# Kernel tuning notes

Hardware: AMD Instinct MI355X
Metric: run time of the kernel (lower is better)

The kernel has to match this reference:

```python
import jax, jax.numpy as jnp
import numpy as np

B, LEN, D, N = 512, 128, 96, 128   # batch, time steps, obs dim, latent dim
NBLOCKS = 5                        # iResNet blocks in encoder/decoder


def expm_fixed(M, squarings=6, order=12):
    """Differentiable matrix exponential: scaling-and-squaring + Taylor-Horner.
    Equivalent to torch.matrix_exp for the well-conditioned skew-symmetric
    A*dt kernels used here (||A*dt|| << 2^squarings)."""
    M = M / (2.0 ** squarings)
    I = jnp.eye(M.shape[-1], dtype=M.dtype)
    P = I
    for k in range(order, 0, -1):  # Horner: I + M(I + M/2(I + ...))
        P = I + (M @ P) / k
    for _ in range(squarings):
        P = P @ P
    return P


def setup_inputs() -> dict:
    key = jax.random.key(0)
    ks = jax.random.split(key, 16)
    # strictly increasing timestamps shared across the batch
    T = jnp.cumsum(0.01 + 0.15 * jax.random.uniform(ks[0], (LEN,), dtype=jnp.float32))
    X = jax.random.normal(ks[1], (B, LEN, D), dtype=jnp.float32)
    mask = jax.random.bernoulli(ks[2], 0.5, (B, LEN, D))  # True = observed
    # skew-symmetric system kernel (kernel_initialization='skew-symmetric')
    W = jax.random.normal(ks[3], (N, N), dtype=jnp.float32) / np.sqrt(N)
    A = 0.5 * (W - W.T)
    # linear embedding d->n and projection n->d
    W_emb = jax.random.normal(ks[4], (N, D), dtype=jnp.float32) / np.sqrt(D)
    b_emb = jnp.zeros((N,), jnp.float32)
    W_proj = jax.random.normal(ks[5], (D, N), dtype=jnp.float32) / np.sqrt(N)
    b_proj = jnp.zeros((D,), jnp.float32)
    # iResNet encoder/decoder: 5 residual blocks of Linear->ReLU->Linear,
    # weights scaled small to mimic the spectral-norm contraction constraint
    cs = 0.5 / np.sqrt(N)
    enc_W1 = jax.random.normal(ks[6], (NBLOCKS, N, N), dtype=jnp.float32) * cs
    enc_b1 = jnp.zeros((NBLOCKS, N), jnp.float32)
    enc_W2 = jax.random.normal(ks[7], (NBLOCKS, N, N), dtype=jnp.float32) * cs
    enc_b2 = jnp.zeros((NBLOCKS, N), jnp.float32)
    dec_W1 = jax.random.normal(ks[8], (NBLOCKS, N, N), dtype=jnp.float32) * cs
    dec_b1 = jnp.zeros((NBLOCKS, N), jnp.float32)
    dec_W2 = jax.random.normal(ks[9], (NBLOCKS, N, N), dtype=jnp.float32) * cs
    dec_b2 = jnp.zeros((NBLOCKS, N), jnp.float32)
    # GRUCell filter: input = concat([xtilde, mask]) (2D features), hidden = D
    s = 1.0 / np.sqrt(D)
    W_ih = jax.random.uniform(ks[10], (3 * D, 2 * D), jnp.float32, -s, s)
    W_hh = jax.random.uniform(ks[11], (3 * D, D), jnp.float32, -s, s)
    b_ih = jax.random.uniform(ks[12], (3 * D,), jnp.float32, -s, s)
    b_hh = jax.random.uniform(ks[13], (3 * D,), jnp.float32, -s, s)
    return {"T": T, "X": X, "mask": mask, "A": A,
            "W_emb": W_emb, "b_emb": b_emb, "W_proj": W_proj, "b_proj": b_proj,
            "enc_W1": enc_W1, "enc_b1": enc_b1, "enc_W2": enc_W2, "enc_b2": enc_b2,
            "dec_W1": dec_W1, "dec_b1": dec_b1, "dec_W2": dec_W2, "dec_b2": dec_b2,
            "W_ih": W_ih, "W_hh": W_hh, "b_ih": b_ih, "b_hh": b_hh}


def reference(T, X, mask, A, W_emb, b_emb, W_proj, b_proj,
              enc_W1, enc_b1, enc_W2, enc_b2,
              dec_W1, dec_b1, dec_W2, dec_b2,
              W_ih, W_hh, b_ih, b_hh):
    def resnet(z, Ws1, bs1, Ws2, bs2):
        for i in range(NBLOCKS):  # fixed small depth
            z = z + jax.nn.relu(z @ Ws1[i].T + bs1[i]) @ Ws2[i].T + bs2[i]
        return z

    def gru(x, h):  # torch.nn.GRUCell math
        gi = x @ W_ih.T + b_ih
        gh = h @ W_hh.T + b_hh
        ir, iz, inn = jnp.split(gi, 3, axis=-1)
        hr, hz, hn = jnp.split(gh, 3, axis=-1)
        r = jax.nn.sigmoid(ir + hr)
        zg = jax.nn.sigmoid(iz + hz)
        ng = jnp.tanh(inn + r * hn)
        return (1.0 - zg) * ng + zg * h

    embed = lambda x: x @ W_emb.T + b_emb
    project = lambda z: z @ W_proj.T + b_proj

    dt = jnp.concatenate([jnp.zeros((1,), T.dtype), jnp.diff(T)])  # (LEN,)
    Xs = jnp.moveaxis(X, 1, 0)      # (LEN, B, D)
    Ms = jnp.moveaxis(mask, 1, 0)   # (LEN, B, D)

    # initial latent state from zero estimate
    z0 = resnet(embed(jnp.zeros((B, D), X.dtype)), enc_W1, enc_b1, enc_W2, enc_b2)

    def step(z, inp):
        dti, xi, mi = inp
        expAdt = expm_fixed(A * dti)                         # (N, N)
        zhat_pre = z @ expAdt.T                              # ODE propagate
        xhat_pre = project(resnet(zhat_pre, dec_W1, dec_b1, dec_W2, dec_b2))
        xtilde = jnp.where(mi, xi, xhat_pre)                 # impute unobserved
        u = jnp.concatenate([xtilde, mi.astype(xi.dtype)], axis=-1)  # concat_mask
        xhat_post = gru(u, xhat_pre)                         # filter update
        z_next = resnet(embed(xhat_post), enc_W1, enc_b1, enc_W2, enc_b2)
        return z_next, xhat_post

    _, Xhat = jax.lax.scan(step, z0, (dt, Xs, Ms))
    return jnp.moveaxis(Xhat, 0, 1)  # (B, LEN, D)
```

## Files before the change

### kernel.cpp

```cpp
#include <hip/hip_runtime.h>
#include <hip/hip_bf16.h>


#define NBATCH 512
#define TLEN 128
#define DDIM 96
#define NDIM 128
#define NBLK 5
#define TAYLOR 8
#define A_STRIDE_E 136

typedef unsigned short u16;
typedef unsigned int u32;

__device__ __forceinline__ float bf2f(u16 u){ union{u32 i; float f;} v; v.i=((u32)u)<<16; return v.f; }
__device__ __forceinline__ float lo2f(u32 w){ union{u32 i; float f;} v; v.i=w<<16; return v.f; }
__device__ __forceinline__ float hi2f(u32 w){ union{u32 i; float f;} v; v.i=w&0xFFFF0000u; return v.f; }
__device__ __forceinline__ u16 f2bf(float x){ union{float f;u32 i;} v; v.f=x; u32 r=v.i+0x7FFF+((v.i>>16)&1); return (u16)(r>>16); }

template<int FM>
__device__ __forceinline__ float ldf(const void* p, int i){
  if constexpr (FM==1) return ((const float*)p)[i];
  else return bf2f(((const u16*)p)[i]);
}

#define OEB1 0
#define OEB2 640
#define ODB1 1280
#define ODB2 1920
#define OBEMB 2560
#define OBPROJ 2688
#define OBIH 2784
#define OBHH 3072
#define NBIAS 3360

struct __align__(16) SMState {
  float e[NDIM];
  float V0[NDIM];
  float V1[NDIM];
  float zh[NDIM];
  float h[NDIM];
  float xpre[DDIM];
  float u[2*DDIM];
  float gi[3*DDIM];
  float gh[3*DDIM];
  float xpost[DDIM];
};

__global__ __launch_bounds__(256, 1)
void expm_kernel(const void* Tp, const void* Ap, u16* Ews)
{
  __shared__ int sf;
  __shared__ __align__(16) u16 Ash2[NDIM*A_STRIDE_E];
  __shared__ __align__(16) float V[2][64*132];
  const int tid = threadIdx.x;
  if (tid==0){
    int all0=1;
    for (int k=0;k<8;k++) all0 &= (((const u32*)Ap)[129*k]==0u);
    sf = all0;
  }
  __syncthreads();
  if (sf) return;

  const int t = blockIdx.x >> 1, half = blockIdx.x & 1;
  float dtv = 0.f;
  if (t>0) dtv = bf2f(((const u16*)Tp)[t]) - bf2f(((const u16*)Tp)[t-1]);
  {
    const uint4* src = (const uint4*)Ap;
    for (int i=tid;i<2048;i+=256){
      const int row=i>>4, c=i&15;
      *(uint4*)((char*)Ash2 + 2*(size_t)row*A_STRIDE_E + 16*c) = src[i];
    }
  }
  const int c2 = tid & 31, rh = tid >> 5;
  const int j0r = rh*16;
  const int lc0 = 2*c2, lc1 = lc0+1;
  const int gc0 = half*64 + lc0, gc1 = gc0+1;

  float acc0[16], acc1[16];
#pragma unroll
  for (int jj=0;jj<16;jj++){
    const int kk = j0r+jj;
    const float i0 = (kk==gc0)?1.f:0.f, i1 = (kk==gc1)?1.f:0.f;
    acc0[jj]=i0; acc1[jj]=i1;
    V[0][lc0*132+kk]=i0; V[0][lc1*132+kk]=i1;
  }
  __syncthreads();
  int cur=0;
#pragma unroll 1
  for (int k=1;k<=8;k++){
    const float sc = dtv/(float)k;
    float o0[16], o1[16];
#pragma unroll
    for (int jj=0;jj<16;jj++){ o0[jj]=0.f; o1[jj]=0.f; }
#pragma unroll 1
    for (int kb=0;kb<16;kb++){
      const float4 va0 = *(const float4*)&V[cur][lc0*132+kb*8];
      const float4 vb0 = *(const float4*)&V[cur][lc0*132+kb*8+4];
      const float4 va1 = *(const float4*)&V[cur][lc1*132+kb*8];
      const float4 vb1 = *(const float4*)&V[cur][lc1*132+kb*8+4];
      const float v0[8]={va0.x,va0.y,va0.z,va0.w,vb0.x,vb0.y,vb0.z,vb0.w};
      const float v1[8]={va1.x,va1.y,va1.z,va1.w,vb1.x,vb1.y,vb1.z,vb1.w};
#pragma unroll
      for (int jj=0;jj<16;jj++){
        const int j = j0r+jj;
        const uint4 w = *(const uint4*)((const char*)Ash2 + 2*(size_t)j*A_STRIDE_E + 16*kb);
        float f;
        f=lo2f(w.x); o0[jj]=fmaf(f,v0[0],o0[jj]); o1[jj]=fmaf(f,v1[0],o1[jj]);
        f=hi2f(w.x); o0[jj]=fmaf(f,v0[1],o0[jj]); o1[jj]=fmaf(f,v1[1],o1[jj]);
        f=lo2f(w.y); o0[jj]=fmaf(f,v0[2],o0[jj]); o1[jj]=fmaf(f,v1[2],o1[jj]);
        f=hi2f(w.y); o0[jj]=fmaf(f,v0[3],o0[jj]); o1[jj]=fmaf(f,v1[3],o1[jj]);
        f=lo2f(w.z); o0[jj]=fmaf(f,v0[4],o0[jj]); o1[jj]=fmaf(f,v1[4],o1[jj]);
        f=hi2f(w.z); o0[jj]=fmaf(f,v0[5],o0[jj]); o1[jj]=fmaf(f,v1[5],o1[jj]);
        f=lo2f(w.w); o0[jj]=fmaf(f,v0[6],o0[jj]); o1[jj]=fmaf(f,v1[6],o1[jj]);
        f=hi2f(w.w); o0[jj]=fmaf(f,v0[7],o0[jj]); o1[jj]=fmaf(f,v1[7],o1[jj]);
      }
    }
    __syncthreads();
#pragma unroll
    for (int jj=0;jj<16;jj++){
      const int j=j0r+jj;
      const float s0=o0[jj]*sc, s1=o1[jj]*sc;
      acc0[jj]+=s0; acc1[jj]+=s1;
      V[cur^1][lc0*132+j]=s0; V[cur^1][lc1*132+j]=s1;
    }
    __syncthreads();
    cur^=1;
  }
#pragma unroll
  for (int jj=0;jj<16;jj++){
    const int j=j0r+jj;
    const u32 pk = (u32)f2bf(acc0[jj]) | ((u32)f2bf(acc1[jj])<<16);
    *((u32*)(Ews + (size_t)t*NDIM*NDIM + (size_t)j*NDIM + gc0)) = pk;
  }
}

template<int FM, int S, int NO, bool WL, class EPI>
__device__ __forceinline__ void mv(const void* __restrict__ Wg, const u16* __restrict__ Wl,
                                   const int ldw, const float* __restrict__ in,
                                   const int kq, const int j0, EPI epi)
{
  constexpr int NC = S/8;
  constexpr int P = (NO+127)/128;
  constexpr bool full = (NO%128==0);
  float a[S];
  {
    const float* p = in + 8*kq;
#pragma unroll
    for (int ci=0; ci<NC; ci++){
      float4 v0 = *(const float4*)(p + 32*ci);
      float4 v1 = *(const float4*)(p + 32*ci + 4);
      a[8*ci+0]=v0.x; a[8*ci+1]=v0.y; a[8*ci+2]=v0.z; a[8*ci+3]=v0.w;
      a[8*ci+4]=v1.x; a[8*ci+5]=v1.y; a[8*ci+6]=v1.z; a[8*ci+7]=v1.w;
    }
  }
#pragma unroll
  for (int pp=0; pp<P; pp++){
    const int j = pp*128 + j0;
    const bool act = full || (j < NO);
    float ac0=0.f, ac1=0.f, ac2=0.f, ac3=0.f;
    if (act){
      if constexpr (WL){
        const char* wr = (const char*)Wl + 2*(size_t)j*A_STRIDE_E + 16*kq;
#pragma unroll
        for (int ci=0; ci<NC; ci++){
          const uint4 w = *(const uint4*)(wr + 64*ci);
          float f;
          f=lo2f(w.x); ac0=fmaf(f,a[8*ci+0],ac0);
          f=hi2f(w.x); ac1=fmaf(f,a[8*ci+1],ac1);
          f=lo2f(w.y); ac2=fmaf(f,a[8*ci+2],ac2);
          f=hi2f(w.y); ac3=fmaf(f,a[8*ci+3],ac3);
          f=lo2f(w.z); ac0=fmaf(f,a[8*ci+4],ac0);
          f=hi2f(w.z); ac1=fmaf(f,a[8*ci+5],ac1);
          f=lo2f(w.w); ac2=fmaf(f,a[8*ci+6],ac2);
          f=hi2f(w.w); ac3=fmaf(f,a[8*ci+7],ac3);
        }
      } else if constexpr (FM==1){
        const float* wr = (const float*)Wg + (size_t)j*ldw + 8*kq;
#pragma unroll
        for (int ci=0; ci<NC; ci++){
          const float4 w0 = *(const float4*)(wr + 32*ci);
          const float4 w1 = *(const float4*)(wr + 32*ci + 4);
          ac0=fmaf(w0.x,a[8*ci+0],ac0); ac1=fmaf(w0.y,a[8*ci+1],ac1);
          ac2=fmaf(w0.z,a[8*ci+2],ac2); ac3=fmaf(w0.w,a[8*ci+3],ac3);
          ac0=fmaf(w1.x,a[8*ci+4],ac0); ac1=fmaf(w1.y,a[8*ci+5],ac1);
          ac2=fmaf(w1.z,a[8*ci+6],ac2); ac3=fmaf(w1.w,a[8*ci+7],ac3);
        }
      } else {
        const u16* wr = (const u16*)Wg + (size_t)j*ldw + 8*kq;
#pragma unroll
        for (int ci=0; ci<NC; ci++){
          const uint4 w = *(const uint4*)(wr + 32*ci);
          float f;
          f=lo2f(w.x); ac0=fmaf(f,a[8*ci+0],ac0);
          f=hi2f(w.x); ac1=fmaf(f,a[8*ci+1],ac1);
          f=lo2f(w.y); ac2=fmaf(f,a[8*ci+2],ac2);
          f=hi2f(w.y); ac3=fmaf(f,a[8*ci+3],ac3);
          f=lo2f(w.z); ac0=fmaf(f,a[8*ci+4],ac0);
          f=hi2f(w.z); ac1=fmaf(f,a[8*ci+5],ac1);
          f=lo2f(w.w); ac2=fmaf(f,a[8*ci+6],ac2);
          f=hi2f(w.w); ac3=fmaf(f,a[8*ci+7],ac3);
        }
      }
    }
    float acc = (ac0+ac1)+(ac2+ac3);
    acc += __shfl_xor(acc,1,64); acc += __shfl_xor(acc,2,64);
    if (act && kq==0) epi(j, acc);
  }
  __syncthreads();
}

template<int FM>
__device__ __forceinline__ void stage_b(const void* src, float* dst, int n, int tid){
  for (int i=tid;i<n;i+=512) dst[i] = ldf<FM>(src,i);
}

template<int FM>
__device__ __forceinline__ void run_all(
    SMState& sm, float* smb, u16* Ash, const int mode, const int useE,
    const void* Tp, const void* Xp, const void* Mp, const void* Ap,
    const void* Wemb, const void* bemb, const void* Wproj, const void* bproj,
    const void* eW1, const void* eb1, const void* eW2, const void* eb2,
    const void* dW1, const void* db1, const void* dW2, const void* db2,
    const void* Wih, const void* Whh, const void* bih, const void* bhh,
    const u16* Ep, void* Out)
{
  const int tid  = threadIdx.x;
  const int lane = tid & 63;
  const int kq   = lane & 3;
  const int j0   = (tid>>6)*16 + (lane>>2);
  const int r0   = blockIdx.x;
  constexpr int WB = NDIM*NDIM*(FM?4:2);

  stage_b<FM>(eb1, smb+OEB1, NBLK*NDIM, tid);
  stage_b<FM>(eb2, smb+OEB2, NBLK*NDIM, tid);
  stage_b<FM>(db1, smb+ODB1, NBLK*NDIM, tid);
  stage_b<FM>(db2, smb+ODB2, NBLK*NDIM, tid);
  stage_b<FM>(bemb, smb+OBEMB, NDIM, tid);
  stage_b<FM>(bproj, smb+OBPROJ, DDIM, tid);
  stage_b<FM>(bih, smb+OBIH, 3*DDIM, tid);
  stage_b<FM>(bhh, smb+OBHH, 3*DDIM, tid);
  if (FM==0 && !useE){
    const uint4* src = (const uint4*)Ap;
    for (int i=tid;i<2048;i+=512){
      const int row=i>>4, c=i&15;
      *(uint4*)((char*)Ash + 2*(size_t)row*A_STRIDE_E + 16*c) = src[i];
    }
  }
  __syncthreads();

  if (tid < NDIM) sm.e[tid] = smb[OBEMB+tid];
  __syncthreads();
#pragma unroll 1
  for (int ib=0; ib<NBLK; ib++){
    const void* W1 = (const char*)eW1 + (size_t)ib*WB;
    const void* W2 = (const char*)eW2 + (size_t)ib*WB;
    const int bo = ib*NDIM;
    mv<FM,32,128,false>(W1, nullptr, NDIM, sm.e, kq, j0, [&](int j,float s){
      sm.h[j]=fmaxf(s+smb[OEB1+bo+j],0.f); });
    mv<FM,32,128,false>(W2, nullptr, NDIM, sm.h, kq, j0, [&](int j,float s){
      sm.e[j]+=s+smb[OEB2+bo+j]; });
  }

#pragma unroll 1
  for (int t=0; t<TLEN; t++){
    float xv_r = 0.f; int m_r = 0;
    if (tid < DDIM){
      const size_t idx = (size_t)r0*TLEN*DDIM + (size_t)t*DDIM + tid;
      if      (mode==0) m_r = ((const u16*)Mp)[idx] != 0;
      else if (mode==1) m_r = ((const u32*)Mp)[idx] != 0;
      else if (mode==2) m_r = ((const unsigned char*)Mp)[idx] != 0;
      else              m_r = ((const int*)Mp)[idx] != 0;
      xv_r = ldf<FM>(Xp, (int)idx);
    }

    if (FM==0 && useE){
      const u16* Et = Ep + (size_t)t*NDIM*NDIM;
      mv<0,32,128,false>(Et, nullptr, NDIM, sm.e, kq, j0, [&](int j,float s){
        sm.zh[j]=s; });
    } else {
      float dtv = 0.f;
      if (t>0) dtv = ldf<FM>(Tp,t) - ldf<FM>(Tp,t-1);
      if (tid < NDIM){ const float z=sm.e[tid]; sm.V0[tid]=z; sm.zh[tid]=z; }
      __syncthreads();
#pragma unroll 1
      for (int k=1;k<=TAYLOR;k++){
        const float sc = dtv/(float)k;
        const float* Vin = (k&1)?sm.V0:sm.V1;
        float*      Vout = (k&1)?sm.V1:sm.V0;
        if constexpr (FM==0){
          mv<0,32,128,true>(nullptr, Ash, NDIM, Vin, kq, j0, [&](int j,float s){
            const float v=s*sc; Vout[j]=v; sm.zh[j]+=v; });
        } else {
          mv<1,32,128,false>(Ap, nullptr, NDIM, Vin, kq, j0, [&](int j,float s){
            const float v=s*sc; Vout[j]=v; sm.zh[j]+=v; });
        }
      }
    }

#pragma unroll 1
    for (int ib=0; ib<NBLK; ib++){
      const void* W1 = (const char*)dW1 + (size_t)ib*WB;
      const void* W2 = (const char*)dW2 + (size_t)ib*WB;
      const int bo = ib*NDIM;
      mv<FM,32,128,false>(W1, nullptr, NDIM, sm.zh, kq, j0, [&](int j,float s){
        sm.h[j]=fmaxf(s+smb[ODB1+bo+j],0.f); });
      mv<FM,32,128,false>(W2, nullptr, NDIM, sm.h, kq, j0, [&](int j,float s){
        sm.zh[j]+=s+smb[ODB2+bo+j]; });
    }

    mv<FM,32,96,false>(Wproj, nullptr, NDIM, sm.zh, kq, j0, [&](int j,float s){
      sm.xpre[j]=s+smb[OBPROJ+j]; });

    if (tid < DDIM){
      sm.u[tid]      = m_r ? xv_r : sm.xpre[tid];
      sm.u[DDIM+tid] = m_r ? 1.f : 0.f;
    }
    __syncthreads();

    mv<FM,48,288,false>(Wih, nullptr, 2*DDIM, sm.u, kq, j0, [&](int j,float s){
      sm.gi[j]=s+smb[OBIH+j]; });
    mv<FM,24,288,false>(Whh, nullptr, DDIM, sm.xpre, kq, j0, [&](int j,float s){
      sm.gh[j]=s+smb[OBHH+j]; });

    if (tid < DDIM){
      const int d = tid;
      const float ir=sm.gi[d], iz=sm.gi[DDIM+d], in_=sm.gi[2*DDIM+d];
      const float hr=sm.gh[d], hz=sm.gh[DDIM+d], hn=sm.gh[2*DDIM+d];
      const float rg = 1.f/(1.f+__expf(-(ir+hr)));
      const float zg = 1.f/(1.f+__expf(-(iz+hz)));
      const float ag = in_ + rg*hn;
      const float e2 = __expf(2.f*ag);
      const float ng = 1.f - 2.f/(e2+1.f);
      const float xp = sm.xpre[d];
      const float xq = (1.f-zg)*ng + zg*xp;
      sm.xpost[d] = xq;
      const size_t idx = (size_t)r0*TLEN*DDIM + (size_t)t*DDIM + d;
      if constexpr (FM==1) ((float*)Out)[idx] = xq;
      else ((__hip_bfloat16*)Out)[idx] = __float2bfloat16(xq);
    }
    __syncthreads();

    mv<FM,24,128,false>(Wemb, nullptr, DDIM, sm.xpost, kq, j0, [&](int j,float s){
      sm.e[j]=s+smb[OBEMB+j]; });

#pragma unroll 1
    for (int ib=0; ib<NBLK; ib++){
      const void* W1 = (const char*)eW1 + (size_t)ib*WB;
      const void* W2 = (const char*)eW2 + (size_t)ib*WB;
      const int bo = ib*NDIM;
      mv<FM,32,128,false>(W1, nullptr, NDIM, sm.e, kq, j0, [&](int j,float s){
        sm.h[j]=fmaxf(s+smb[OEB1+bo+j],0.f); });
      mv<FM,32,128,false>(W2, nullptr, NDIM, sm.h, kq, j0, [&](int j,float s){
        sm.e[j]+=s+smb[OEB2+bo+j]; });
    }
  }
}

__global__ __launch_bounds__(512, 4)
void linode_kernel(const void* Tp, const void* Xp, const void* Mp, const void* Ap,
                   const void* Wemb, const void* bemb, const void* Wproj, const void* bproj,
                   const void* eW1, const void* eb1, const void* eW2, const void* eb2,
                   const void* dW1, const void* db1, const void* dW2, const void* db2,
                   const void* Wih, const void* Whh, const void* bih, const void* bhh,
                   const u16* Ep, const int useE, void* Out)
{
  __shared__ SMState sm;
  __shared__ float smb[NBIAS];
  __shared__ __align__(16) u16 Ash[NDIM*A_STRIDE_E];
  __shared__ int s_f[4];
  const int tid = threadIdx.x;

  if (tid < 4) s_f[tid] = 0;
  __syncthreads();
  if (tid == 0){
    int all0 = 1;
    for (int k=0;k<8;k++) all0 &= (((const u32*)Ap)[129*k] == 0u);
    s_f[3] = all0;
  }
  {
    const u32* mw = (const u32*)Mp;
    int fb=0, ff=0, fg=0;
    for (int i=tid;i<2048;i+=512){
      const u32 w = mw[i];
      if (w == 0x3F803F80u) fb = 1;
      if ((w&0xFFFFu)==0x3F80u || (w>>16)==0x3F80u) ff = 1;
      if (w > 1u) fg = 1;
    }
    if (fb) atomicOr(&s_f[0],1);
    if (ff) atomicOr(&s_f[1],1);
    if (fg) atomicOr(&s_f[2],1);
  }
  __syncthreads();
  const int mode = s_f[0] ? 0 : (s_f[1] ? 1 : (s_f[2] ? 2 : 3));
  const int f32m = s_f[3];
  __syncthreads();

  if (f32m)
    run_all<1>(sm, smb, Ash, mode, useE, Tp, Xp, Mp, Ap, Wemb, bemb, Wproj, bproj,
               eW1, eb1, eW2, eb2, dW1, db1, dW2, db2, Wih, Whh, bih, bhh, Ep, Out);
  else
    run_all<0>(sm, smb, Ash, mode, useE, Tp, Xp, Mp, Ap, Wemb, bemb, Wproj, bproj,
               eW1, eb1, eW2, eb2, dW1, db1, dW2, db2, Wih, Whh, bih, bhh, Ep, Out);
}

extern "C" void kernel_launch(void* const* d_in, const int* in_sizes, int n_in,
                              void* d_out, int out_size, void* d_ws, size_t ws_size,
                              hipStream_t stream)
{
  (void)in_sizes; (void)n_in; (void)out_size;
  const int useE = (ws_size >= (size_t)TLEN*NDIM*NDIM*2) ? 1 : 0;
  if (useE)
    hipLaunchKernelGGL(expm_kernel, dim3(2*TLEN), dim3(256), 0, stream,
                       d_in[0], d_in[3], (u16*)d_ws);
  hipLaunchKernelGGL(linode_kernel, dim3(NBATCH), dim3(512), 0, stream,
                     d_in[0], d_in[1], d_in[2], d_in[3],
                     d_in[4], d_in[5], d_in[6], d_in[7],
                     d_in[8], d_in[9], d_in[10], d_in[11],
                     d_in[12], d_in[13], d_in[14], d_in[15],
                     d_in[16], d_in[17], d_in[18], d_in[19],
                     (const u16*)d_ws, useE, d_out);
}
```

Before: 5.207 ms.

## Add software-pipelined bf16 path that prefetches next layer weights into registers

Adds a dedicated run_pipe path for bf16 inputs with the precomputed expm workspace. Inside each per-step chain of matvecs it loads the next layer's weight fragment into registers while the current dot product and reduction run, hiding global/L2 load latency behind compute. The GRU gate matvecs are computed directly with several outputs per thread, and the bias staging moves ahead of the path dispatch. This costs extra registers and duplicated code, and it assumes bf16 weights and a workspace large enough for the expm buffer.

```diff
diff --git a/kernel.cpp b/kernel.cpp
--- a/kernel.cpp
+++ b/kernel.cpp
@@ -132,6 +132,216 @@
     const int j=j0r+jj;
     const u32 pk = (u32)f2bf(acc0[jj]) | ((u32)f2bf(acc1[jj])<<16);
     *((u32*)(Ews + (size_t)t*NDIM*NDIM + (size_t)j*NDIM + gc0)) = pk;
+  }
+}
+
+template<int NC>
+__device__ __forceinline__ void wload(uint4* wp, const u16* W, int ldw_e, int j, int kq){
+  const u16* wr = W + (size_t)j*ldw_e + 8*kq;
+#pragma unroll
+  for (int ci=0; ci<NC; ci++) wp[ci] = *(const uint4*)(wr + 32*ci);
+}
+template<int S>
+__device__ __forceinline__ void aload(float* a, const float* in, int kq){
+  const float* p = in + 8*kq;
+#pragma unroll
+  for (int ci=0; ci<S/8; ci++){
+    float4 v0 = *(const float4*)(p + 32*ci);
+    float4 v1 = *(const float4*)(p + 32*ci + 4);
+    a[8*ci+0]=v0.x; a[8*ci+1]=v0.y; a[8*ci+2]=v0.z; a[8*ci+3]=v0.w;
+    a[8*ci+4]=v1.x; a[8*ci+5]=v1.y; a[8*ci+6]=v1.z; a[8*ci+7]=v1.w;
+  }
+}
+template<int NC>
+__device__ __forceinline__ float dotw(const uint4* wp, const float* a){
+  float ac0=0.f,ac1=0.f,ac2=0.f,ac3=0.f;
+#pragma unroll
+  for (int ci=0; ci<NC; ci++){
+    const uint4 w = wp[ci]; float f;
+    f=lo2f(w.x); ac0=fmaf(f,a[8*ci+0],ac0);
+    f=hi2f(w.x); ac1=fmaf(f,a[8*ci+1],ac1);
+    f=lo2f(w.y); ac2=fmaf(f,a[8*ci+2],ac2);
+    f=hi2f(w.y); ac3=fmaf(f,a[8*ci+3],ac3);
+    f=lo2f(w.z); ac0=fmaf(f,a[8*ci+4],ac0);
+    f=hi2f(w.z); ac1=fmaf(f,a[8*ci+5],ac1);
+    f=lo2f(w.w); ac2=fmaf(f,a[8*ci+6],ac2);
+    f=hi2f(w.w); ac3=fmaf(f,a[8*ci+7],ac3);
+  }
+  return (ac0+ac1)+(ac2+ac3);
+}
+template<int NC>
+__device__ __forceinline__ float dotl(const u16* W, int ldw_e, int j, int kq, const float* a){
+  uint4 wl[NC]; wload<NC>(wl,W,ldw_e,j,kq); return dotw<NC>(wl,a);
+}
+__device__ __forceinline__ float red4(float x){
+  x += __shfl_xor(x,1,64); x += __shfl_xor(x,2,64); return x;
+}
+
+__device__ __forceinline__ void run_pipe(
+    SMState& sm, float* smb, const int mode,
+    const void* Xp, const void* Mp,
+    const u16* Wemb, const u16* Wproj,
+    const u16* eW1, const u16* eW2,
+    const u16* dW1, const u16* dW2,
+    const u16* Wih, const u16* Whh,
+    const u16* Ep, __hip_bfloat16* Out)
+{
+  const int tid  = threadIdx.x;
+  const int lane = tid & 63;
+  const int kq   = lane & 3;
+  const int j0   = (tid>>6)*16 + (lane>>2);
+  const int r0   = blockIdx.x;
+  const bool epl = (kq==0);
+
+  if (tid < NDIM) sm.e[tid] = smb[OBEMB+tid];
+  __syncthreads();
+  {
+    float a[32];
+#pragma unroll 1
+    for (int ib=0; ib<NBLK; ib++){
+      aload<32>(a, sm.e, kq);
+      float acc = red4(dotl<4>(eW1+ib*NDIM*NDIM, NDIM, j0, kq, a));
+      if (epl) sm.h[j0]=fmaxf(acc+smb[OEB1+ib*NDIM+j0],0.f);
+      __syncthreads();
+      aload<32>(a, sm.h, kq);
+      acc = red4(dotl<4>(eW2+ib*NDIM*NDIM, NDIM, j0, kq, a));
+      if (epl) sm.e[j0]+=acc+smb[OEB2+ib*NDIM+j0];
+      __syncthreads();
+    }
+  }
+
+  uint4 wp[6];
+  wload<4>(wp, Ep, NDIM, j0, kq);
+
+#pragma unroll 1
+  for (int t=0; t<TLEN; t++){
+    float xv_r = 0.f; int m_r = 0;
+    if (epl && j0 < DDIM){
+      const size_t idx = (size_t)r0*TLEN*DDIM + (size_t)t*DDIM + j0;
+      if      (mode==0) m_r = ((const u16*)Mp)[idx] != 0;
+      else if (mode==1) m_r = ((const u32*)Mp)[idx] != 0;
+      else if (mode==2) m_r = ((const unsigned char*)Mp)[idx] != 0;
+      else              m_r = ((const int*)Mp)[idx] != 0;
+      xv_r = bf2f(((const u16*)Xp)[idx]);
+    }
+
+    {
+      float a[32]; aload<32>(a, sm.e, kq);
+      float acc = dotw<4>(wp, a);
+      wload<4>(wp, dW1, NDIM, j0, kq);
+      acc = red4(acc);
+      if (epl) sm.zh[j0] = acc;
+    }
+    __syncthreads();
+
+#pragma unroll 1
+    for (int ib=0; ib<NBLK; ib++){
+      float a[32];
+      aload<32>(a, sm.zh, kq);
+      float acc = dotw<4>(wp, a);
+      wload<4>(wp, dW2+ib*NDIM*NDIM, NDIM, j0, kq);
+      acc = red4(acc);
+      if (epl) sm.h[j0]=fmaxf(acc+smb[ODB1+ib*NDIM+j0],0.f);
+      __syncthreads();
+      aload<32>(a, sm.h, kq);
+      acc = dotw<4>(wp, a);
+      if (ib<NBLK-1) wload<4>(wp, dW1+(ib+1)*NDIM*NDIM, NDIM, j0, kq);
+      else           wload<4>(wp, Wproj, NDIM, (j0<DDIM?j0:DDIM-1), kq);
+      acc = red4(acc);
+      if (epl) sm.zh[j0]+=acc+smb[ODB2+ib*NDIM+j0];
+      __syncthreads();
+    }
+
+    {
+      float a[32]; aload<32>(a, sm.zh, kq);
+      float acc = dotw<4>(wp, a);
+      wload<6>(wp, Wih, 2*DDIM, j0, kq);
+      acc = red4(acc);
+      if (epl && j0 < DDIM){
+        const float xp = acc + smb[OBPROJ+j0];
+        sm.xpre[j0] = xp;
+        sm.u[j0]      = m_r ? xv_r : xp;
+        sm.u[DDIM+j0] = m_r ? 1.f : 0.f;
+      }
+    }
+    __syncthreads();
+
+    {
+      float a[48]; aload<48>(a, sm.u, kq);
+      float g0 = dotw<6>(wp, a);
+      wload<3>(wp, Whh, DDIM, j0, kq);
+      float g1 = dotl<6>(Wih, 2*DDIM, 128+j0, kq, a);
+      float g2 = (j0<32) ? dotl<6>(Wih, 2*DDIM, 256+j0, kq, a) : 0.f;
+      g0=red4(g0); g1=red4(g1); g2=red4(g2);
+      if (epl){
+        sm.gi[j0]     = g0 + smb[OBIH+j0];
+        sm.gi[128+j0] = g1 + smb[OBIH+128+j0];
+        if (j0<32) sm.gi[256+j0] = g2 + smb[OBIH+256+j0];
+      }
+    }
+    __syncthreads();
+
+    {
+      float a[24]; aload<24>(a, sm.xpre, kq);
+      float g0 = dotw<3>(wp, a);
+      wload<3>(wp, Wemb, DDIM, j0, kq);
+      float g1 = dotl<3>(Whh, DDIM, 128+j0, kq, a);
+      float g2 = (j0<32) ? dotl<3>(Whh, DDIM, 256+j0, kq, a) : 0.f;
+      g0=red4(g0); g1=red4(g1); g2=red4(g2);
+      if (epl){
+        sm.gh[j0]     = g0 + smb[OBHH+j0];
+        sm.gh[128+j0] = g1 + smb[OBHH+128+j0];
+        if (j0<32) sm.gh[256+j0] = g2 + smb[OBHH+256+j0];
+      }
+    }
+    __syncthreads();
+
+    if (tid < DDIM){
+      const int d = tid;
+      const float ir=sm.gi[d], iz=sm.gi[DDIM+d], in_=sm.gi[2*DDIM+d];
+      const float hr=sm.gh[d], hz=sm.gh[DDIM+d], hn=sm.gh[2*DDIM+d];
+      const float rg = 1.f/(1.f+__expf(-(ir+hr)));
+      const float zg = 1.f/(1.f+__expf(-(iz+hz)));
+      const float ag = in_ + rg*hn;
+      const float e2 = __expf(2.f*ag);
+      const float ng = 1.f - 2.f/(e2+1.f);
+      const float xp = sm.xpre[d];
+      const float xq = (1.f-zg)*ng + zg*xp;
+      sm.xpost[d] = xq;
+      const size_t idx = (size_t)r0*TLEN*DDIM + (size_t)t*DDIM + d;
+      Out[idx] = __float2bfloat16(xq);
+    }
+    __syncthreads();
+
+    {
+      float a[24]; aload<24>(a, sm.xpost, kq);
+      float acc = dotw<3>(wp, a);
+      wload<4>(wp, eW1, NDIM, j0, kq);
+      acc = red4(acc);
+      if (epl) sm.e[j0] = acc + smb[OBEMB+j0];
+    }
+    __syncthreads();
+
+#pragma unroll 1
+    for (int ib=0; ib<NBLK; ib++){
+      float a[32];
+      aload<32>(a, sm.e, kq);
+      float acc = dotw<4>(wp, a);
+      wload<4>(wp, eW2+ib*NDIM*NDIM, NDIM, j0, kq);
+      acc = red4(acc);
+      if (epl) sm.h[j0]=fmaxf(acc+smb[OEB1+ib*NDIM+j0],0.f);
+      __syncthreads();
+      aload<32>(a, sm.h, kq);
+      acc = dotw<4>(wp, a);
+      if (ib<NBLK-1) wload<4>(wp, eW1+(ib+1)*NDIM*NDIM, NDIM, j0, kq);
+      else {
+        const u16* En = Ep + (size_t)((t+1<TLEN)?(t+1):t)*NDIM*NDIM;
+        wload<4>(wp, En, NDIM, j0, kq);
+      }
+      acc = red4(acc);
+      if (epl) sm.e[j0]+=acc+smb[OEB2+ib*NDIM+j0];
+      __syncthreads();
+    }
   }
 }
 
@@ -217,13 +427,13 @@
 
 template<int FM>
 __device__ __forceinline__ void run_all(
-    SMState& sm, float* smb, u16* Ash, const int mode, const int useE,
+    SMState& sm, float* smb, u16* Ash, const int mode,
     const void* Tp, const void* Xp, const void* Mp, const void* Ap,
     const void* Wemb, const void* bemb, const void* Wproj, const void* bproj,
     const void* eW1, const void* eb1, const void* eW2, const void* eb2,
     const void* dW1, const void* db1, const void* dW2, const void* db2,
     const void* Wih, const void* Whh, const void* bih, const void* bhh,
-    const u16* Ep, void* Out)
+    void* Out)
 {
   const int tid  = threadIdx.x;
   const int lane = tid & 63;
@@ -232,15 +442,7 @@
   const int r0   = blockIdx.x;
   constexpr int WB = NDIM*NDIM*(FM?4:2);
 
-  stage_b<FM>(eb1, smb+OEB1, NBLK*NDIM, tid);
-  stage_b<FM>(eb2, smb+OEB2, NBLK*NDIM, tid);
-  stage_b<FM>(db1, smb+ODB1, NBLK*NDIM, tid);
-  stage_b<FM>(db2, smb+ODB2, NBLK*NDIM, tid);
-  stage_b<FM>(bemb, smb+OBEMB, NDIM, tid);
-  stage_b<FM>(bproj, smb+OBPROJ, DDIM, tid);
-  stage_b<FM>(bih, smb+OBIH, 3*DDIM, tid);
-  stage_b<FM>(bhh, smb+OBHH, 3*DDIM, tid);
-  if (FM==0 && !useE){
+  if (FM==0){
     const uint4* src = (const uint4*)Ap;
     for (int i=tid;i<2048;i+=512){
       const int row=i>>4, c=i&15;
@@ -274,11 +476,7 @@
       xv_r = ldf<FM>(Xp, (int)idx);
     }
 
-    if (FM==0 && useE){
-      const u16* Et = Ep + (size_t)t*NDIM*NDIM;
-      mv<0,32,128,false>(Et, nullptr, NDIM, sm.e, kq, j0, [&](int j,float s){
-        sm.zh[j]=s; });
-    } else {
+    {
       float dtv = 0.f;
       if (t>0) dtv = ldf<FM>(Tp,t) - ldf<FM>(Tp,t-1);
       if (tid < NDIM){ const float z=sm.e[tid]; sm.V0[tid]=z; sm.zh[tid]=z; }
@@ -396,12 +594,47 @@
   const int f32m = s_f[3];
   __syncthreads();
 
-  if (f32m)
-    run_all<1>(sm, smb, Ash, mode, useE, Tp, Xp, Mp, Ap, Wemb, bemb, Wproj, bproj,
-               eW1, eb1, eW2, eb2, dW1, db1, dW2, db2, Wih, Whh, bih, bhh, Ep, Out);
-  else
-    run_all<0>(sm, smb, Ash, mode, useE, Tp, Xp, Mp, Ap, Wemb, bemb, Wproj, bproj,
-               eW1, eb1, eW2, eb2, dW1, db1, dW2, db2, Wih, Whh, bih, bhh, Ep, Out);
+  if (!f32m && useE){
+    stage_b<0>(eb1, smb+OEB1, NBLK*NDIM, tid);
+    stage_b<0>(eb2, smb+OEB2, NBLK*NDIM, tid);
+    stage_b<0>(db1, smb+ODB1, NBLK*NDIM, tid);
+    stage_b<0>(db2, smb+ODB2, NBLK*NDIM, tid);
+    stage_b<0>(bemb, smb+OBEMB, NDIM, tid);
+    stage_b<0>(bproj, smb+OBPROJ, DDIM, tid);
+    stage_b<0>(bih, smb+OBIH, 3*DDIM, tid);
+    stage_b<0>(bhh, smb+OBHH, 3*DDIM, tid);
+    __syncthreads();
+    run_pipe(sm, smb, mode, Xp, Mp,
+             (const u16*)Wemb, (const u16*)Wproj,
+             (const u16*)eW1, (const u16*)eW2,
+             (const u16*)dW1, (const u16*)dW2,
+             (const u16*)Wih, (const u16*)Whh,
+             Ep, (__hip_bfloat16*)Out);
+  } else if (f32m){
+    stage_b<1>(eb1, smb+OEB1, NBLK*NDIM, tid);
+    stage_b<1>(eb2, smb+OEB2, NBLK*NDIM, tid);
+    stage_b<1>(db1, smb+ODB1, NBLK*NDIM, tid);
+    stage_b<1>(db2, smb+ODB2, NBLK*NDIM, tid);
+    stage_b<1>(bemb, smb+OBEMB, NDIM, tid);
+    stage_b<1>(bproj, smb+OBPROJ, DDIM, tid);
+    stage_b<1>(bih, smb+OBIH, 3*DDIM, tid);
+    stage_b<1>(bhh, smb+OBHH, 3*DDIM, tid);
+    __syncthreads();
+    run_all<1>(sm, smb, Ash, mode, Tp, Xp, Mp, Ap, Wemb, bemb, Wproj, bproj,
+               eW1, eb1, eW2, eb2, dW1, db1, dW2, db2, Wih, Whh, bih, bhh, Out);
+  } else {
+    stage_b<0>(eb1, smb+OEB1, NBLK*NDIM, tid);
+    stage_b<0>(eb2, smb+OEB2, NBLK*NDIM, tid);
+    stage_b<0>(db1, smb+ODB1, NBLK*NDIM, tid);
+    stage_b<0>(db2, smb+ODB2, NBLK*NDIM, tid);
+    stage_b<0>(bemb, smb+OBEMB, NDIM, tid);
+    stage_b<0>(bproj, smb+OBPROJ, DDIM, tid);
+    stage_b<0>(bih, smb+OBIH, 3*DDIM, tid);
+    stage_b<0>(bhh, smb+OBHH, 3*DDIM, tid);
+    __syncthreads();
+    run_all<0>(sm, smb, Ash, mode, Tp, Xp, Mp, Ap, Wemb, bemb, Wproj, bproj,
+               eW1, eb1, eW2, eb2, dW1, db1, dW2, db2, Wih, Whh, bih, bhh, Out);
+  }
 }
 
 extern "C" void kernel_launch(void* const* d_in, const int* in_sizes, int n_in,
```

Result: no change. 5.194 ms (-0.2%).
